# Optimization experiments

Measured on AMD Instinct MI355X. Metric: run time of the kernel, lower is better.

Reference implementation:

```python
import jax, jax.numpy as jnp
import numpy as np

B, N = 32, 128
V, P, L = 50000, 40, 50
WD, UD = 100, 25
D = WD + UD          # 125: LSTM hidden per direction
H2 = 2 * D           # 250: BiLSTM output
HID = 100            # hidden_dim for scorers


def setup_inputs() -> dict:
    key = jax.random.key(0)
    ks = iter(jax.random.split(key, 40))
    p = lambda shape: jax.random.normal(next(ks), shape, jnp.float32) * 0.05
    inp = {
        'word_ids': jax.random.randint(next(ks), (B, N), 0, V),
        'upos_ids': jax.random.randint(next(ks), (B, N), 0, P),
        'target_arcs': jax.random.randint(next(ks), (B, N), 0, N),
        'wlookup': p((V, WD)),
        'tlookup': p((V, UD)),  # original sizes tag table by word_count
        # LSTM layer 0 (input D=125), layer 1 (input 2D=250); f=fwd, b=bwd dir
        'l0f_Wih': p((4 * D, D)), 'l0f_Whh': p((4 * D, D)), 'l0f_b': p((4 * D,)),
        'l0b_Wih': p((4 * D, D)), 'l0b_Whh': p((4 * D, D)), 'l0b_b': p((4 * D,)),
        'l1f_Wih': p((4 * D, H2)), 'l1f_Whh': p((4 * D, D)), 'l1f_b': p((4 * D,)),
        'l1b_Wih': p((4 * D, H2)), 'l1b_Whh': p((4 * D, D)), 'l1b_b': p((4 * D,)),
        'eh_W': p((HID, H2)), 'eh_b': p((HID,)),
        'em_W': p((HID, H2)), 'em_b': p((HID,)),
        'es_W': p((1, HID)), 'es_b': p((1,)),
        'lh_W': p((HID, H2)), 'lh_b': p((HID,)),
        'lm_W': p((HID, H2)), 'lm_b': p((HID,)),
        'ls_W': p((L, HID)), 'ls_b': p((L,)),
    }
    return inp


def _lstm_dir(x, Wih, Whh, b, reverse):
    # x: [B,T,in] -> h: [B,T,H], pytorch gate order i,f,g,o
    H = Whh.shape[1]
    xg = jnp.einsum('bti,gi->btg', x, Wih) + b  # precompute input projections

    def step(carry, xt):
        h, c = carry
        g = xt + h @ Whh.T
        i, f, gg, o = jnp.split(g, 4, axis=-1)
        c = jax.nn.sigmoid(f) * c + jax.nn.sigmoid(i) * jnp.tanh(gg)
        h = jax.nn.sigmoid(o) * jnp.tanh(c)
        return (h, c), h

    h0 = jnp.zeros((x.shape[0], H), x.dtype)
    _, hs = jax.lax.scan(step, (h0, h0), jnp.swapaxes(xg, 0, 1), reverse=reverse)
    return jnp.swapaxes(hs, 0, 1)


def _bilstm(x, Wf, Uf, bf, Wb, Ub, bb):
    return jnp.concatenate([_lstm_dir(x, Wf, Uf, bf, False),
                            _lstm_dir(x, Wb, Ub, bb, True)], axis=-1)


def reference(word_ids, upos_ids, target_arcs, wlookup, tlookup,
              l0f_Wih, l0f_Whh, l0f_b, l0b_Wih, l0b_Whh, l0b_b,
              l1f_Wih, l1f_Whh, l1f_b, l1b_Wih, l1b_Whh, l1b_b,
              eh_W, eh_b, em_W, em_b, es_W, es_b,
              lh_W, lh_b, lm_W, lm_b, ls_W, ls_b):
    n = word_ids.shape[1]
    words = jnp.concatenate([wlookup[word_ids], tlookup[upos_ids]], axis=-1)  # [B,N,125]
    h0 = _bilstm(words, l0f_Wih, l0f_Whh, l0f_b, l0b_Wih, l0b_Whh, l0b_b)
    word_exprs = _bilstm(h0, l1f_Wih, l1f_Whh, l1f_b, l1b_Wih, l1b_Whh, l1b_b)  # [B,N,250]

    word_h = word_exprs @ eh_W.T + eh_b  # [B,N,100]
    word_m = word_exprs @ em_W.T + em_b
    # fused pairwise biaffine-style scoring (replaces the O(n) python loop)
    pair = jnp.tanh(word_h[:, :, None, :] + word_m[:, None, :, :])  # [B,N,N,100]
    arc_scores = jnp.einsum('bijh,h->bij', pair, es_W[0]) + es_b[0]  # [B,N,N]

    # training path: margin augmentation
    target_arcs = target_arcs.at[:, 0].set(0)
    margin = 1.0 - jax.nn.one_hot(target_arcs, n, dtype=arc_scores.dtype)
    arc_scores = arc_scores + margin

    # decode() is an external MST decoder; greedy argmax stand-in
    parsed_trees = jnp.argmax(arc_scores, axis=-1)

    tree = target_arcs  # is_train path
    rel_heads = jnp.take_along_axis(word_exprs, tree[:, :, None], axis=1)  # [B,N,250]
    rel_heads = rel_heads @ lh_W.T + lh_b
    rel_mod = word_exprs @ lm_W.T + lm_b
    rel_scores = jnp.tanh(rel_mod + rel_heads) @ ls_W.T + ls_b  # [B,N,L]
    predicted_rels = jnp.argmax(rel_scores, axis=-1)
    return (parsed_trees, predicted_rels, arc_scores, rel_scores)
```

## Files before the change

### kernel.cpp

```cpp
#include <hip/hip_runtime.h>
#include <hip/hip_bf16.h>
#include <math.h>

#define B 32
#define N 128
#define BT (B*N)
#define WD 100
#define UD 25
#define D 125
#define G4 (4*D)
#define H2 (2*D)
#define HID 100
#define L 50

__device__ __forceinline__ float fast_tanh(float x) {
    float e = __expf(2.0f * x);
    return 1.0f - 2.0f / (e + 1.0f);
}
__device__ __forceinline__ float fast_sigmoid(float x) {
    return 1.0f / (1.0f + __expf(-x));
}
__device__ __forceinline__ float bcast_lane(float v, int k) {
    return __builtin_bit_cast(float, __builtin_amdgcn_readlane(__builtin_bit_cast(int, v), k));
}

struct TJob { const float* src; float* dst; int R, C, ldo, coff, tile0, tiles_x; };
struct TArgs { TJob j[12]; };

__global__ __launch_bounds__(256)
void setup_fused(TArgs a, int n_tr,
                 const int* __restrict__ wids, const int* __restrict__ uids,
                 const float* __restrict__ wl, const float* __restrict__ tl,
                 float* __restrict__ words,
                 const float* __restrict__ l0f_b, const float* __restrict__ l0b_b,
                 const float* __restrict__ l1f_b, const float* __restrict__ l1b_b,
                 const float* __restrict__ eh_b, const float* __restrict__ em_b,
                 const float* __restrict__ lm_b,
                 float* __restrict__ b_l0, float* __restrict__ b_l1,
                 float* __restrict__ b_s3,
                 float* __restrict__ p0, float* __restrict__ p1,
                 float* __restrict__ p2, float* __restrict__ p3) {
    __shared__ float tile[32][33];
    int bid = blockIdx.x;
    int tid = threadIdx.x;
    if (bid < n_tr) {
        int ji = 0;
        #pragma unroll
        for (int i = 1; i < 12; i++) if (bid >= a.j[i].tile0) ji = i;
        TJob jb = a.j[ji];
        int t = bid - jb.tile0;
        int tx = t % jb.tiles_x, ty = t / jb.tiles_x;
        int txx = tid & 31, tyy = tid >> 5;
        int k0 = tx*32, n0 = ty*32;
        #pragma unroll
        for (int dy = 0; dy < 32; dy += 8) {
            int n = n0 + tyy + dy, k = k0 + txx;
            if (n < jb.R && k < jb.C)
                tile[tyy+dy][txx] = jb.src[(size_t)n*jb.C + k];
        }
        __syncthreads();
        #pragma unroll
        for (int dy = 0; dy < 32; dy += 8) {
            int k = k0 + tyy + dy, n = n0 + txx;
            if (k < jb.C && n < jb.R)
                jb.dst[(size_t)k*jb.ldo + jb.coff + n] = tile[txx][tyy+dy];
        }
        return;
    }
    bid -= n_tr;
    if (bid < 2048) {
        int bt = bid*2 + (tid >> 7);
        int t = tid & 127;
        int wid = wids[bt], uid = uids[bt];
        if (t < WD)       words[bt*D + t] = wl[(size_t)wid*WD + t];
        else if (t < D)   words[bt*D + t] = tl[(size_t)uid*UD + (t - WD)];
        return;
    }
    bid -= 2048;
    if (bid < 9) {
        int t = bid*256 + tid;
        if (t < 500)        b_l0[t] = l0f_b[t];
        else if (t < 1000)  b_l0[t] = l0b_b[t-500];
        else if (t < 1500)  b_l1[t-1000] = l1f_b[t-1000];
        else if (t < 2000)  b_l1[t-1000] = l1b_b[t-1500];
        else if (t < 2100)  b_s3[t-2000] = eh_b[t-2000];
        else if (t < 2200)  b_s3[t-2000] = em_b[t-2100];
        else if (t < 2300)  b_s3[t-2000] = lm_b[t-2200];
        return;
    }
    bid -= 9;
    int e = bid*256 + tid;
    if (e < 12144) {
        int m = e / 3036, o = e % 3036;
        float* p = (m == 0) ? p0 : (m == 1) ? p1 : (m == 2) ? p2 : p3;
        if (o < 1500) {
            int k = o / 12, cc = 500 + (o % 12);
            p[k*512 + cc] = 0.0f;
        } else {
            int o2 = o - 1500;
            p[(125 + (o2 >> 9))*512 + (o2 & 511)] = 0.0f;
        }
    }
}

#define MT 16
template<int CPT, int BD>
__device__ __forceinline__
void proj_body(const float* __restrict__ x, const float* __restrict__ WT,
               const float* __restrict__ bias, float* __restrict__ out,
               int Ncols, int K, int ldx, const int* __restrict__ gather_idx,
               int blk, float* xs) {
    int m0 = blk * MT;
    for (int e = threadIdx.x; e < MT * K; e += BD) {
        int r = e / K, k = e - r * K;
        int m = m0 + r;
        int row = m;
        if (gather_idx) {
            int bb = m >> 7, np = m & 127;
            row = (bb << 7) + (np == 0 ? 0 : gather_idx[m]);
        }
        xs[k*17 + r] = x[(size_t)row*ldx + k];
    }
    __syncthreads();
    int n0 = threadIdx.x;
    int lane = threadIdx.x & 63;
    float acc[CPT][MT];
    int ncl[CPT];
    #pragma unroll
    for (int j = 0; j < CPT; j++) {
        int n = n0 + j*BD;
        ncl[j] = (n < Ncols) ? n : (Ncols - 1);
        #pragma unroll
        for (int r = 0; r < MT; r++) acc[j][r] = 0.0f;
    }
    float wkc[4][CPT];
    #pragma unroll
    for (int q = 0; q < 4; q++)
        #pragma unroll
        for (int j = 0; j < CPT; j++)
            wkc[q][j] = WT[(size_t)q*Ncols + ncl[j]];
    int k0 = 0;
    for (; k0 + 8 <= K; k0 += 4) {
        float xv = xs[(k0 + (lane >> 4))*17 + (lane & 15)];
        float wkn[4][CPT];
        #pragma unroll
        for (int q = 0; q < 4; q++)
            #pragma unroll
            for (int j = 0; j < CPT; j++)
                wkn[q][j] = WT[(size_t)(k0 + 4 + q)*Ncols + ncl[j]];
        #pragma unroll
        for (int q = 0; q < 4; q++) {
            #pragma unroll
            for (int r = 0; r < 16; r++) {
                float hv = bcast_lane(xv, q*16 + r);
                #pragma unroll
                for (int j = 0; j < CPT; j++)
                    acc[j][r] = fmaf(wkc[q][j], hv, acc[j][r]);
            }
        }
        #pragma unroll
        for (int q = 0; q < 4; q++)
            #pragma unroll
            for (int j = 0; j < CPT; j++)
                wkc[q][j] = wkn[q][j];
    }
    {
        float xv = xs[(k0 + (lane >> 4))*17 + (lane & 15)];
        #pragma unroll
        for (int q = 0; q < 4; q++) {
            #pragma unroll
            for (int r = 0; r < 16; r++) {
                float hv = bcast_lane(xv, q*16 + r);
                #pragma unroll
                for (int j = 0; j < CPT; j++)
                    acc[j][r] = fmaf(wkc[q][j], hv, acc[j][r]);
            }
        }
        k0 += 4;
    }
    for (; k0 < K; k0++) {
        float xv = xs[k0*17 + (lane & 15)];
        float wk[CPT];
        #pragma unroll
        for (int j = 0; j < CPT; j++) wk[j] = WT[(size_t)k0*Ncols + ncl[j]];
        #pragma unroll
        for (int r = 0; r < 16; r++) {
            float hv = bcast_lane(xv, r);
            #pragma unroll
            for (int j = 0; j < CPT; j++)
                acc[j][r] = fmaf(wk[j], hv, acc[j][r]);
        }
    }
    #pragma unroll
    for (int j = 0; j < CPT; j++) {
        int n = n0 + j*BD;
        if (n < Ncols) {
            float bb = bias[n];
            #pragma unroll
            for (int r = 0; r < MT; r++) out[(size_t)(m0 + r)*Ncols + n] = acc[j][r] + bb;
        }
    }
}

__global__ __launch_bounds__(512)
void proj_t(const float* __restrict__ x, const float* __restrict__ WT,
            const float* __restrict__ bias, float* __restrict__ out,
            int Ncols, int K, int ldx) {
    __shared__ float xs[250 * 17 + 16];
    proj_body<2, 512>(x, WT, bias, out, Ncols, K, ldx, nullptr, blockIdx.x, xs);
}

__global__ __launch_bounds__(256)
void proj_s3lh(const float* __restrict__ x,
               const float* __restrict__ WTa, const float* __restrict__ ba,
               float* __restrict__ outa,
               const float* __restrict__ WTb, const float* __restrict__ bb,
               float* __restrict__ outb, const int* __restrict__ gather_idx) {
    __shared__ float xs[250 * 17 + 16];
    int job = blockIdx.x >> 8;
    int blk = blockIdx.x & 255;
    if (job == 0)
        proj_body<2, 256>(x, WTa, ba, outa, 300, H2, H2, nullptr, blk, xs);
    else
        proj_body<2, 256>(x, WTb, bb, outb, 100, H2, H2, gather_idx, blk, xs);
}

__global__ __launch_bounds__(512)
void lstm_scan(const float* __restrict__ xgc,
               const float* __restrict__ WhTf, const float* __restrict__ WhTb,
               float* __restrict__ out) {
    int dir = blockIdx.x & 1;
    int b = blockIdx.x >> 1;
    const float* WhT = dir ? WhTb : WhTf;
    int off = dir ? D : 0;
    int t = threadIdx.x;
    int lane = t & 63;
    int w = t >> 6;
    int ks = w >> 1;
    int cg = ((w & 1) << 6) + lane;
    int c0 = cg << 2;

    __shared__ __align__(16) float hbuf[128];
    __shared__ __align__(16) float pbuf[4*512];

    float4 wv[32];
    #pragma unroll
    for (int k = 0; k < 32; k++)
        wv[k] = *(const float4*)&WhT[(size_t)(ks*32 + k)*512 + c0];

    if (t < 128) hbuf[t] = 0.0f;
    __syncthreads();

    const float* xb = xgc + (size_t)b * N * 1000 + dir * 500;
    bool xa = (ks == 0) && (cg < 125);
    float4 x_next = make_float4(0.f, 0.f, 0.f, 0.f);
    if (xa) x_next = *(const float4*)&xb[(size_t)(dir ? (N-1) : 0)*1000 + c0];

    float c = 0.0f;
    for (int ti = 0; ti < N; ti++) {
        int tt = dir ? (N-1-ti) : ti;
        float vh = hbuf[ks*32 + (lane & 31)];
        float4 x_cur = x_next;
        float4 xn = make_float4(0.f, 0.f, 0.f, 0.f);
        if (xa && ti + 1 < N)
            xn = *(const float4*)&xb[(size_t)(dir ? (tt-1) : (tt+1))*1000 + c0];
        float a0 = x_cur.x, a1 = x_cur.y, a2 = x_cur.z, a3 = x_cur.w;
        #pragma unroll
        for (int k = 0; k < 32; k++) {
            float hs = bcast_lane(vh, k);
            a0 = fmaf(wv[k].x, hs, a0);
            a1 = fmaf(wv[k].y, hs, a1);
            a2 = fmaf(wv[k].z, hs, a2);
            a3 = fmaf(wv[k].w, hs, a3);
        }
        x_next = xn;
        *(float4*)&pbuf[ks*512 + c0] = make_float4(a0, a1, a2, a3);
        __syncthreads();
        if (t < D) {
            float iv = pbuf[t]       + pbuf[512+t]       + pbuf[1024+t]       + pbuf[1536+t];
            float fv = pbuf[125+t]   + pbuf[512+125+t]   + pbuf[1024+125+t]   + pbuf[1536+125+t];
            float gv = pbuf[250+t]   + pbuf[512+250+t]   + pbuf[1024+250+t]   + pbuf[1536+250+t];
            float ov = pbuf[375+t]   + pbuf[512+375+t]   + pbuf[1024+375+t]   + pbuf[1536+375+t];
            float si = fast_sigmoid(iv);
            float sf = fast_sigmoid(fv);
            float so = fast_sigmoid(ov);
            c = sf * c + si * fast_tanh(gv);
            float h = so * fast_tanh(c);
            hbuf[t] = h;
            out[(size_t)(b*N + tt)*H2 + off + t] = h;
        }
        __syncthreads();
    }
}

#define ITILE 4
__global__ __launch_bounds__(128)
void arc_rel(const float* __restrict__ s3,
             const float* __restrict__ esW, const float* __restrict__ esb,
             const int* __restrict__ ta, const float* __restrict__ rh,
             const float* __restrict__ lsW, const float* __restrict__ lsb,
             float* __restrict__ arc_out, float* __restrict__ tree_out,
             float* __restrict__ rel_out, float* __restrict__ pred_out) {
    __shared__ float wms[128 * 101];
    __shared__ float whs[ITILE][HID];
    __shared__ float es[HID];
    __shared__ float sv[128];
    __shared__ int   si[128];
    int j = threadIdx.x;

    if (blockIdx.x < 1024) {
        int blk = blockIdx.x;
        int b = blk >> 5, it = blk & 31;
        for (int e = j; e < 128 * HID; e += 128) {
            int r = e / HID, h = e - r * HID;
            wms[r*101 + h] = s3[(size_t)(b*N + r)*300 + 100 + h];
        }
        for (int e = j; e < ITILE * HID; e += 128) {
            int ii = e / HID, h = e - ii * HID;
            whs[ii][h] = s3[(size_t)(b*N + it*ITILE + ii)*300 + h];
        }
        if (j < HID) es[j] = esW[j];
        __syncthreads();
        float eb = esb[0];
        const float* wmr = &wms[j * 101];
        for (int ii = 0; ii < ITILE; ii++) {
            int i = it * ITILE + ii;
            int bi = b * N + i;
            float acc = 0.0f;
            for (int h = 0; h < HID; h++)
                acc = fmaf(es[h], fast_tanh(whs[ii][h] + wmr[h]), acc);
            int tai = (i == 0) ? 0 : ta[bi];
            float score = acc + eb + 1.0f - ((j == tai) ? 1.0f : 0.0f);
            arc_out[(size_t)bi*N + j] = score;
            sv[j] = score; si[j] = j;
            __syncthreads();
            for (int s = 64; s; s >>= 1) {
                if (j < s) {
                    float ov = sv[j+s]; int oi = si[j+s];
                    if (ov > sv[j] || (ov == sv[j] && oi < si[j])) { sv[j] = ov; si[j] = oi; }
                }
                __syncthreads();
            }
            if (j == 0) tree_out[bi] = (float)si[0];
            __syncthreads();
        }
    } else {
        int bt = blockIdx.x - 1024;
        float* tv = es;
        if (j < HID)
            tv[j] = fast_tanh(s3[(size_t)bt*300 + 200 + j] + rh[(size_t)bt*HID + j]);
        __syncthreads();
        float score = -1e30f;
        if (j < L) {
            float acc = 0.0f;
            const float* wrow = lsW + j*HID;
            for (int h = 0; h < HID; h++) acc = fmaf(wrow[h], tv[h], acc);
            score = acc + lsb[j];
            rel_out[(size_t)bt*L + j] = score;
        }
        sv[j] = score; si[j] = j;
        __syncthreads();
        for (int s = 64; s; s >>= 1) {
            if (j < s) {
                float ov = sv[j+s]; int oi = si[j+s];
                if (ov > sv[j] || (ov == sv[j] && oi < si[j])) { sv[j] = ov; si[j] = oi; }
            }
            __syncthreads();
        }
        if (j == 0) pred_out[bt] = (float)si[0];
    }
}

extern "C" void kernel_launch(void* const* d_in, const int* in_sizes, int n_in,
                              void* d_out, int out_size, void* d_ws, size_t ws_size,
                              hipStream_t stream) {
    const int*   word_ids    = (const int*)  d_in[0];
    const int*   upos_ids    = (const int*)  d_in[1];
    const int*   target_arcs = (const int*)  d_in[2];
    const float* wlookup     = (const float*)d_in[3];
    const float* tlookup     = (const float*)d_in[4];
    const float* l0f_Wih = (const float*)d_in[5];
    const float* l0f_Whh = (const float*)d_in[6];
    const float* l0f_b   = (const float*)d_in[7];
    const float* l0b_Wih = (const float*)d_in[8];
    const float* l0b_Whh = (const float*)d_in[9];
    const float* l0b_b   = (const float*)d_in[10];
    const float* l1f_Wih = (const float*)d_in[11];
    const float* l1f_Whh = (const float*)d_in[12];
    const float* l1f_b   = (const float*)d_in[13];
    const float* l1b_Wih = (const float*)d_in[14];
    const float* l1b_Whh = (const float*)d_in[15];
    const float* l1b_b   = (const float*)d_in[16];
    const float* eh_W = (const float*)d_in[17];
    const float* eh_b = (const float*)d_in[18];
    const float* em_W = (const float*)d_in[19];
    const float* em_b = (const float*)d_in[20];
    const float* es_W = (const float*)d_in[21];
    const float* es_b = (const float*)d_in[22];
    const float* lh_W = (const float*)d_in[23];
    const float* lh_b = (const float*)d_in[24];
    const float* lm_W = (const float*)d_in[25];
    const float* lm_b = (const float*)d_in[26];
    const float* ls_W = (const float*)d_in[27];
    const float* ls_b = (const float*)d_in[28];

    float* out = (float*)d_out;
    float* trees_out = out;
    float* preds_out = out + BT;
    float* arc_out   = out + 2*BT;
    float* rel_out   = out + 2*BT + BT*N;

    float* ws = (float*)d_ws;
    float* A       = ws;
    float* words   = ws + 4096000;
    float* C       = ws + 4608000;
    float* WT_l0   = ws + 5632000;
    float* WT_l1   = ws + 5757000;
    float* WT_s3   = ws + 6007000;
    float* WT_lh   = ws + 6082000;
    float* WhT_l0f = ws + 6107000;
    float* WhT_l0b = ws + 6172536;
    float* WhT_l1f = ws + 6238072;
    float* WhT_l1b = ws + 6303608;
    float* b_l0    = ws + 6369144;
    float* b_l1    = ws + 6370144;
    float* b_s3    = ws + 6371144;
    float* rel_head = ws + 6372144;

    TArgs ta{};
    int n_tr = 0;
    {
        auto tiles = [](int R, int C_) { return ((C_+31)/32) * ((R+31)/32); };
        struct { const float* s; float* d; int R, C, ldo, coff; } js[12] = {
            { l0f_Wih, WT_l0, 500, 125, 1000, 0 },
            { l0b_Wih, WT_l0, 500, 125, 1000, 500 },
            { l1f_Wih, WT_l1, 500, 250, 1000, 0 },
            { l1b_Wih, WT_l1, 500, 250, 1000, 500 },
            { eh_W, WT_s3, 100, 250, 300, 0 },
            { em_W, WT_s3, 100, 250, 300, 100 },
            { lm_W, WT_s3, 100, 250, 300, 200 },
            { lh_W, WT_lh, 100, 250, 100, 0 },
            { l0f_Whh, WhT_l0f, 500, 125, 512, 0 },
            { l0b_Whh, WhT_l0b, 500, 125, 512, 0 },
            { l1f_Whh, WhT_l1f, 500, 125, 512, 0 },
            { l1b_Whh, WhT_l1b, 500, 125, 512, 0 },
        };
        for (int i = 0; i < 12; i++) {
            ta.j[i].src = js[i].s;  ta.j[i].dst = js[i].d;
            ta.j[i].R = js[i].R;    ta.j[i].C = js[i].C;
            ta.j[i].ldo = js[i].ldo; ta.j[i].coff = js[i].coff;
            ta.j[i].tile0 = n_tr;
            ta.j[i].tiles_x = (js[i].C + 31) / 32;
            n_tr += tiles(js[i].R, js[i].C);
        }
    }
    setup_fused<<<n_tr + 2048 + 9 + 48, 256, 0, stream>>>(
        ta, n_tr, word_ids, upos_ids, wlookup, tlookup, words,
        l0f_b, l0b_b, l1f_b, l1b_b, eh_b, em_b, lm_b,
        b_l0, b_l1, b_s3, WhT_l0f, WhT_l0b, WhT_l1f, WhT_l1b);

    proj_t<<<BT/MT, 512, 0, stream>>>(words, WT_l0, b_l0, A, 1000, D, D);

    lstm_scan<<<B*2, 512, 0, stream>>>(A, WhT_l0f, WhT_l0b, C);

    proj_t<<<BT/MT, 512, 0, stream>>>(C, WT_l1, b_l1, A, 1000, H2, H2);

    lstm_scan<<<B*2, 512, 0, stream>>>(A, WhT_l1f, WhT_l1b, C);

    proj_s3lh<<<512, 256, 0, stream>>>(C, WT_s3, b_s3, A,
                                       WT_lh, lh_b, rel_head, target_arcs);

    arc_rel<<<1024 + BT, 128, 0, stream>>>(A, es_W, es_b, target_arcs, rel_head,
                                           ls_W, ls_b, arc_out, trees_out,
                                           rel_out, preds_out);
}
```

Before: 558.2 us.

## Compute LSTM cell redundantly per wave to drop second barrier and hbuf round-trip

Each wave now computes the gate nonlinearities for its own 32-element slice of h directly from a double-buffered partial-sum buffer, keeping h in a register instead of writing it to shared memory. This removes one of the two block barriers per timestep and the hbuf store/load. The input projection prefetch is also deepened to two steps ahead, and the launch bounds request two blocks per CU. The trade-off is redundant cell computation across wave pairs, and the occupancy hint could force register spills given the 128-float weight cache per thread.

```diff
diff --git a/kernel.cpp b/kernel.cpp
--- a/kernel.cpp
+++ b/kernel.cpp
@@ -225,7 +225,7 @@
         proj_body<2, 256>(x, WTb, bb, outb, 100, H2, H2, gather_idx, blk, xs);
 }
 
-__global__ __launch_bounds__(512)
+__global__ __launch_bounds__(512, 2)
 void lstm_scan(const float* __restrict__ xgc,
                const float* __restrict__ WhTf, const float* __restrict__ WhTb,
                float* __restrict__ out) {
@@ -240,30 +240,37 @@
     int cg = ((w & 1) << 6) + lane;
     int c0 = cg << 2;
 
-    __shared__ __align__(16) float hbuf[128];
-    __shared__ __align__(16) float pbuf[4*512];
+    __shared__ __align__(16) float pbuf[2][4*512];
 
     float4 wv[32];
     #pragma unroll
     for (int k = 0; k < 32; k++)
         wv[k] = *(const float4*)&WhT[(size_t)(ks*32 + k)*512 + c0];
 
-    if (t < 128) hbuf[t] = 0.0f;
-    __syncthreads();
-
     const float* xb = xgc + (size_t)b * N * 1000 + dir * 500;
     bool xa = (ks == 0) && (cg < 125);
-    float4 x_next = make_float4(0.f, 0.f, 0.f, 0.f);
-    if (xa) x_next = *(const float4*)&xb[(size_t)(dir ? (N-1) : 0)*1000 + c0];
-
-    float c = 0.0f;
+    float4 zero4 = make_float4(0.f, 0.f, 0.f, 0.f);
+    float4 xA = zero4, xB = zero4;
+    if (xa) {
+        xA = *(const float4*)&xb[(size_t)(dir ? (N-1) : 0)*1000 + c0];
+        xB = *(const float4*)&xb[(size_t)(dir ? (N-2) : 1)*1000 + c0];
+    }
+
+    int t4 = ks*32 + (lane & 31);
+    bool act = (lane < 32) && (t4 < 125);
+    bool sto = act && ((w & 1) == 0);
+
+    float vh = 0.0f;
+    float c  = 0.0f;
+
     for (int ti = 0; ti < N; ti++) {
         int tt = dir ? (N-1-ti) : ti;
-        float vh = hbuf[ks*32 + (lane & 31)];
-        float4 x_cur = x_next;
-        float4 xn = make_float4(0.f, 0.f, 0.f, 0.f);
-        if (xa && ti + 1 < N)
-            xn = *(const float4*)&xb[(size_t)(dir ? (tt-1) : (tt+1))*1000 + c0];
+        float4 x_cur = xA;
+        float4 xC = zero4;
+        if (xa && ti + 2 < N) {
+            int tn = dir ? (tt-2) : (tt+2);
+            xC = *(const float4*)&xb[(size_t)tn*1000 + c0];
+        }
         float a0 = x_cur.x, a1 = x_cur.y, a2 = x_cur.z, a3 = x_cur.w;
         #pragma unroll
         for (int k = 0; k < 32; k++) {
@@ -273,23 +280,26 @@
             a2 = fmaf(wv[k].z, hs, a2);
             a3 = fmaf(wv[k].w, hs, a3);
         }
-        x_next = xn;
-        *(float4*)&pbuf[ks*512 + c0] = make_float4(a0, a1, a2, a3);
-        __syncthreads();
-        if (t < D) {
-            float iv = pbuf[t]       + pbuf[512+t]       + pbuf[1024+t]       + pbuf[1536+t];
-            float fv = pbuf[125+t]   + pbuf[512+125+t]   + pbuf[1024+125+t]   + pbuf[1536+125+t];
-            float gv = pbuf[250+t]   + pbuf[512+250+t]   + pbuf[1024+250+t]   + pbuf[1536+250+t];
-            float ov = pbuf[375+t]   + pbuf[512+375+t]   + pbuf[1024+375+t]   + pbuf[1536+375+t];
+        xA = xB; xB = xC;
+        float* pb = &pbuf[ti & 1][0];
+        *(float4*)&pb[ks*512 + c0] = make_float4(a0, a1, a2, a3);
+        asm volatile("s_waitcnt lgkmcnt(0)" ::: "memory");
+        __builtin_amdgcn_s_barrier();
+        asm volatile("" ::: "memory");
+        if (act) {
+            float iv = pb[t4]       + pb[512+t4]       + pb[1024+t4]       + pb[1536+t4];
+            float fv = pb[125+t4]   + pb[512+125+t4]   + pb[1024+125+t4]   + pb[1536+125+t4];
+            float gv = pb[250+t4]   + pb[512+250+t4]   + pb[1024+250+t4]   + pb[1536+250+t4];
+            float ov = pb[375+t4]   + pb[512+375+t4]   + pb[1024+375+t4]   + pb[1536+375+t4];
             float si = fast_sigmoid(iv);
             float sf = fast_sigmoid(fv);
             float so = fast_sigmoid(ov);
             c = sf * c + si * fast_tanh(gv);
             float h = so * fast_tanh(c);
-            hbuf[t] = h;
-            out[(size_t)(b*N + tt)*H2 + off + t] = h;
-        }
-        __syncthreads();
+            vh = h;
+            if (sto)
+                out[(size_t)(b*N + tt)*H2 + off + t4] = h;
+        }
     }
 }
 
```

After: 576.5 us. 3.3% more time.

## Store LSTM recurrent weights as packed fp16 and use dot2 accumulation

Applied to the files above, without the earlier changes.

The recurrent weight matrices are converted in the setup kernel into packed fp16 pairs laid out along k, replacing the fp32 transpose jobs. The scan kernel now re-reads these packed weights from global/L2 memory at every timestep instead of holding 32 float4 registers, uses fdot2 with broadcast packed hidden values, prefetches inputs two steps ahead, and replaces __syncthreads with a raw barrier plus an lgkm wait. This lowers register pressure and halves the multiply-add instruction count on the serial recurrence. In exchange, each step reloads the weights from cache and the recurrence loses precision through fp16 rounding of h and W.

```diff
diff --git a/kernel.cpp b/kernel.cpp
--- a/kernel.cpp
+++ b/kernel.cpp
@@ -1,5 +1,6 @@
 #include <hip/hip_runtime.h>
 #include <hip/hip_bf16.h>
+#include <hip/hip_fp16.h>
 #include <math.h>
 
 #define B 32
@@ -23,9 +24,33 @@
 __device__ __forceinline__ float bcast_lane(float v, int k) {
     return __builtin_bit_cast(float, __builtin_amdgcn_readlane(__builtin_bit_cast(int, v), k));
 }
+__device__ __forceinline__ unsigned bcast_lane_u(unsigned v, int k) {
+    return (unsigned)__builtin_amdgcn_readlane((int)v, k);
+}
+
+__device__ __forceinline__ unsigned pack_f16x2(float lo, float hi) {
+    __half hl = __float2half_rn(lo), hh = __float2half_rn(hi);
+    unsigned a = (unsigned)__builtin_bit_cast(unsigned short, hl);
+    unsigned b = (unsigned)__builtin_bit_cast(unsigned short, hh);
+    return a | (b << 16);
+}
+
+typedef _Float16 h2_t __attribute__((ext_vector_type(2)));
+__device__ __forceinline__ float dot2acc(unsigned wu, unsigned hu, float acc) {
+#if __has_builtin(__builtin_amdgcn_fdot2)
+    return __builtin_amdgcn_fdot2(__builtin_bit_cast(h2_t, wu),
+                                  __builtin_bit_cast(h2_t, hu), acc, false);
+#else
+    h2_t wv = __builtin_bit_cast(h2_t, wu);
+    h2_t hv = __builtin_bit_cast(h2_t, hu);
+    acc = fmaf((float)wv[0], (float)hv[0], acc);
+    acc = fmaf((float)wv[1], (float)hv[1], acc);
+    return acc;
+#endif
+}
 
 struct TJob { const float* src; float* dst; int R, C, ldo, coff, tile0, tiles_x; };
-struct TArgs { TJob j[12]; };
+struct TArgs { TJob j[8]; };
 
 __global__ __launch_bounds__(256)
 void setup_fused(TArgs a, int n_tr,
@@ -38,15 +63,17 @@
                  const float* __restrict__ lm_b,
                  float* __restrict__ b_l0, float* __restrict__ b_l1,
                  float* __restrict__ b_s3,
-                 float* __restrict__ p0, float* __restrict__ p1,
-                 float* __restrict__ p2, float* __restrict__ p3) {
+                 const float* __restrict__ s0, const float* __restrict__ s1,
+                 const float* __restrict__ s2, const float* __restrict__ s3w,
+                 unsigned* __restrict__ d0, unsigned* __restrict__ d1,
+                 unsigned* __restrict__ d2, unsigned* __restrict__ d3) {
     __shared__ float tile[32][33];
     int bid = blockIdx.x;
     int tid = threadIdx.x;
     if (bid < n_tr) {
         int ji = 0;
         #pragma unroll
-        for (int i = 1; i < 12; i++) if (bid >= a.j[i].tile0) ji = i;
+        for (int i = 1; i < 8; i++) if (bid >= a.j[i].tile0) ji = i;
         TJob jb = a.j[ji];
         int t = bid - jb.tile0;
         int tx = t % jb.tiles_x, ty = t / jb.tiles_x;
@@ -90,17 +117,19 @@
     }
     bid -= 9;
     int e = bid*256 + tid;
-    if (e < 12144) {
-        int m = e / 3036, o = e % 3036;
-        float* p = (m == 0) ? p0 : (m == 1) ? p1 : (m == 2) ? p2 : p3;
-        if (o < 1500) {
-            int k = o / 12, cc = 500 + (o % 12);
-            p[k*512 + cc] = 0.0f;
-        } else {
-            int o2 = o - 1500;
-            p[(125 + (o2 >> 9))*512 + (o2 & 511)] = 0.0f;
-        }
-    }
+    int m = e >> 15;
+    int r = e & 32767;
+    int pk = r >> 9;
+    int g  = r & 511;
+    const float* s = (m == 0) ? s0 : (m == 1) ? s1 : (m == 2) ? s2 : s3w;
+    unsigned* dd   = (m == 0) ? d0 : (m == 1) ? d1 : (m == 2) ? d2 : d3;
+    float v0 = 0.0f, v1 = 0.0f;
+    if (g < 500) {
+        int k0 = pk << 1;
+        if (k0 < 125)     v0 = s[(size_t)g*125 + k0];
+        if (k0 + 1 < 125) v1 = s[(size_t)g*125 + k0 + 1];
+    }
+    dd[(pk << 9) + g] = pack_f16x2(v0, v1);
 }
 
 #define MT 16
@@ -225,13 +254,13 @@
         proj_body<2, 256>(x, WTb, bb, outb, 100, H2, H2, gather_idx, blk, xs);
 }
 
-__global__ __launch_bounds__(512)
+__global__ __launch_bounds__(512, 2)
 void lstm_scan(const float* __restrict__ xgc,
-               const float* __restrict__ WhTf, const float* __restrict__ WhTb,
+               const unsigned* __restrict__ WhHf, const unsigned* __restrict__ WhHb,
                float* __restrict__ out) {
     int dir = blockIdx.x & 1;
     int b = blockIdx.x >> 1;
-    const float* WhT = dir ? WhTb : WhTf;
+    const unsigned* WhH = dir ? WhHb : WhHf;
     int off = dir ? D : 0;
     int t = threadIdx.x;
     int lane = t & 63;
@@ -243,39 +272,49 @@
     __shared__ __align__(16) float hbuf[128];
     __shared__ __align__(16) float pbuf[4*512];
 
-    float4 wv[32];
-    #pragma unroll
-    for (int k = 0; k < 32; k++)
-        wv[k] = *(const float4*)&WhT[(size_t)(ks*32 + k)*512 + c0];
+    const unsigned* wp = WhH + (size_t)(ks*16)*512 + c0;
+
+    const float* xb = xgc + (size_t)b * N * 1000 + dir * 500;
+    bool xa = (ks == 0) && (cg < 125);
+    float4 zero4 = make_float4(0.f, 0.f, 0.f, 0.f);
+    float4 xA = zero4, xB = zero4;
+    if (xa) {
+        xA = *(const float4*)&xb[(size_t)(dir ? (N-1) : 0)*1000 + c0];
+        xB = *(const float4*)&xb[(size_t)(dir ? (N-2) : 1)*1000 + c0];
+    }
 
     if (t < 128) hbuf[t] = 0.0f;
     __syncthreads();
-
-    const float* xb = xgc + (size_t)b * N * 1000 + dir * 500;
-    bool xa = (ks == 0) && (cg < 125);
-    float4 x_next = make_float4(0.f, 0.f, 0.f, 0.f);
-    if (xa) x_next = *(const float4*)&xb[(size_t)(dir ? (N-1) : 0)*1000 + c0];
 
     float c = 0.0f;
     for (int ti = 0; ti < N; ti++) {
         int tt = dir ? (N-1-ti) : ti;
-        float vh = hbuf[ks*32 + (lane & 31)];
-        float4 x_cur = x_next;
-        float4 xn = make_float4(0.f, 0.f, 0.f, 0.f);
-        if (xa && ti + 1 < N)
-            xn = *(const float4*)&xb[(size_t)(dir ? (tt-1) : (tt+1))*1000 + c0];
+        uint4 wq[16];
+        #pragma unroll
+        for (int p = 0; p < 16; p++)
+            wq[p] = *(const uint4*)&wp[(size_t)p*512];
+        float2 h2 = *(const float2*)&hbuf[ks*32 + ((lane & 15) << 1)];
+        unsigned vhp = pack_f16x2(h2.x, h2.y);
+        float4 x_cur = xA;
+        float4 xC = zero4;
+        if (xa && ti + 2 < N) {
+            int tn = dir ? (tt-2) : (tt+2);
+            xC = *(const float4*)&xb[(size_t)tn*1000 + c0];
+        }
         float a0 = x_cur.x, a1 = x_cur.y, a2 = x_cur.z, a3 = x_cur.w;
         #pragma unroll
-        for (int k = 0; k < 32; k++) {
-            float hs = bcast_lane(vh, k);
-            a0 = fmaf(wv[k].x, hs, a0);
-            a1 = fmaf(wv[k].y, hs, a1);
-            a2 = fmaf(wv[k].z, hs, a2);
-            a3 = fmaf(wv[k].w, hs, a3);
-        }
-        x_next = xn;
+        for (int p = 0; p < 16; p++) {
+            unsigned hp = bcast_lane_u(vhp, p);
+            a0 = dot2acc(wq[p].x, hp, a0);
+            a1 = dot2acc(wq[p].y, hp, a1);
+            a2 = dot2acc(wq[p].z, hp, a2);
+            a3 = dot2acc(wq[p].w, hp, a3);
+        }
+        xA = xB; xB = xC;
         *(float4*)&pbuf[ks*512 + c0] = make_float4(a0, a1, a2, a3);
-        __syncthreads();
+        asm volatile("s_waitcnt lgkmcnt(0)" ::: "memory");
+        __builtin_amdgcn_s_barrier();
+        asm volatile("" ::: "memory");
         if (t < D) {
             float iv = pbuf[t]       + pbuf[512+t]       + pbuf[1024+t]       + pbuf[1536+t];
             float fv = pbuf[125+t]   + pbuf[512+125+t]   + pbuf[1024+125+t]   + pbuf[1536+125+t];
@@ -289,7 +328,9 @@
             hbuf[t] = h;
             out[(size_t)(b*N + tt)*H2 + off + t] = h;
         }
-        __syncthreads();
+        asm volatile("s_waitcnt lgkmcnt(0)" ::: "memory");
+        __builtin_amdgcn_s_barrier();
+        asm volatile("" ::: "memory");
     }
 }
 
@@ -418,20 +459,20 @@
     float* WT_l1   = ws + 5757000;
     float* WT_s3   = ws + 6007000;
     float* WT_lh   = ws + 6082000;
-    float* WhT_l0f = ws + 6107000;
-    float* WhT_l0b = ws + 6172536;
-    float* WhT_l1f = ws + 6238072;
-    float* WhT_l1b = ws + 6303608;
-    float* b_l0    = ws + 6369144;
-    float* b_l1    = ws + 6370144;
-    float* b_s3    = ws + 6371144;
-    float* rel_head = ws + 6372144;
+    unsigned* WhH_l0f = (unsigned*)(ws + 6107000);
+    unsigned* WhH_l0b = (unsigned*)(ws + 6139768);
+    unsigned* WhH_l1f = (unsigned*)(ws + 6172536);
+    unsigned* WhH_l1b = (unsigned*)(ws + 6205304);
+    float* b_l0    = ws + 6238072;
+    float* b_l1    = ws + 6239072;
+    float* b_s3    = ws + 6240072;
+    float* rel_head = ws + 6241072;
 
     TArgs ta{};
     int n_tr = 0;
     {
         auto tiles = [](int R, int C_) { return ((C_+31)/32) * ((R+31)/32); };
-        struct { const float* s; float* d; int R, C, ldo, coff; } js[12] = {
+        struct { const float* s; float* d; int R, C, ldo, coff; } js[8] = {
             { l0f_Wih, WT_l0, 500, 125, 1000, 0 },
             { l0b_Wih, WT_l0, 500, 125, 1000, 500 },
             { l1f_Wih, WT_l1, 500, 250, 1000, 0 },
@@ -440,12 +481,8 @@
             { em_W, WT_s3, 100, 250, 300, 100 },
             { lm_W, WT_s3, 100, 250, 300, 200 },
             { lh_W, WT_lh, 100, 250, 100, 0 },
-            { l0f_Whh, WhT_l0f, 500, 125, 512, 0 },
-            { l0b_Whh, WhT_l0b, 500, 125, 512, 0 },
-            { l1f_Whh, WhT_l1f, 500, 125, 512, 0 },
-            { l1b_Whh, WhT_l1b, 500, 125, 512, 0 },
         };
-        for (int i = 0; i < 12; i++) {
+        for (int i = 0; i < 8; i++) {
             ta.j[i].src = js[i].s;  ta.j[i].dst = js[i].d;
             ta.j[i].R = js[i].R;    ta.j[i].C = js[i].C;
             ta.j[i].ldo = js[i].ldo; ta.j[i].coff = js[i].coff;
@@ -454,18 +491,20 @@
             n_tr += tiles(js[i].R, js[i].C);
         }
     }
-    setup_fused<<<n_tr + 2048 + 9 + 48, 256, 0, stream>>>(
+    setup_fused<<<n_tr + 2048 + 9 + 512, 256, 0, stream>>>(
         ta, n_tr, word_ids, upos_ids, wlookup, tlookup, words,
         l0f_b, l0b_b, l1f_b, l1b_b, eh_b, em_b, lm_b,
-        b_l0, b_l1, b_s3, WhT_l0f, WhT_l0b, WhT_l1f, WhT_l1b);
+        b_l0, b_l1, b_s3,
+        l0f_Whh, l0b_Whh, l1f_Whh, l1b_Whh,
+        WhH_l0f, WhH_l0b, WhH_l1f, WhH_l1b);
 
     proj_t<<<BT/MT, 512, 0, stream>>>(words, WT_l0, b_l0, A, 1000, D, D);
 
-    lstm_scan<<<B*2, 512, 0, stream>>>(A, WhT_l0f, WhT_l0b, C);
+    lstm_scan<<<B*2, 512, 0, stream>>>(A, WhH_l0f, WhH_l0b, C);
 
     proj_t<<<BT/MT, 512, 0, stream>>>(C, WT_l1, b_l1, A, 1000, H2, H2);
 
-    lstm_scan<<<B*2, 512, 0, stream>>>(A, WhT_l1f, WhT_l1b, C);
+    lstm_scan<<<B*2, 512, 0, stream>>>(A, WhH_l1f, WhH_l1b, C);
 
     proj_s3lh<<<512, 256, 0, stream>>>(C, WT_s3, b_s3, A,
                                        WT_lh, lh_b, rel_head, target_arcs);
```

New measurement: 534.2 us. 1.04x faster.
